# Kernel tuning notes

Hardware: AMD Instinct MI355X
Metric: run time of the kernel (lower is better)

The kernel has to match this reference:

```python
import jax, jax.numpy as jnp
import numpy as np

N = 500_000   # total nodes
D = 256       # in_dim
G = 1024      # num graphs (segments)
H = max(32, D // 2)  # gate hidden = 128
L = D // 2    # local pool dim = 128


def setup_inputs() -> dict:
    key = jax.random.key(0)
    ks = jax.random.split(key, 8)
    x = jax.random.normal(ks[0], (N, D), dtype=jnp.float32)
    batch = jnp.sort(jax.random.randint(ks[1], (N,), 0, G, dtype=jnp.int32))
    s = 0.02
    w1 = jax.random.normal(ks[2], (D, H), dtype=jnp.float32) * s
    b1 = jnp.zeros((H,), dtype=jnp.float32)
    w2 = jax.random.normal(ks[3], (H, 1), dtype=jnp.float32) * s
    b2 = jnp.zeros((1,), dtype=jnp.float32)
    lp_w = jax.random.normal(ks[4], (D, L), dtype=jnp.float32) * s
    lp_b = jnp.zeros((L,), dtype=jnp.float32)
    return {"x": x, "batch": batch, "w1": w1, "b1": b1, "w2": w2,
            "b2": b2, "lp_w": lp_w, "lp_b": lp_b}


def reference(x, batch, w1, b1, w2, b2, lp_w, lp_b):
    # segment counts (guard empty segments)
    ones = jnp.ones((x.shape[0],), dtype=x.dtype)
    cnt = jax.ops.segment_sum(ones, batch, num_segments=G)
    cnt = jnp.maximum(cnt, 1.0)[:, None]                      # [G,1]

    # mean pool
    mean_p = jax.ops.segment_sum(x, batch, num_segments=G) / cnt

    # max pool
    max_p = jax.ops.segment_max(x, batch, num_segments=G)

    # global attention pool: gate MLP -> per-segment softmax -> weighted sum
    # (Dropout is identity at inference.)
    h = jax.nn.gelu(x @ w1 + b1, approximate=False)           # [N,H]
    gate = (h @ w2 + b2)[:, 0]                                # [N]
    gmax = jax.ops.segment_max(gate, batch, num_segments=G)   # [G]
    e = jnp.exp(gate - gmax[batch])                           # [N]
    denom = jax.ops.segment_sum(e, batch, num_segments=G)     # [G]
    a = e / denom[batch]                                      # [N] softmax per graph
    att_p = jax.ops.segment_sum(a[:, None] * x, batch, num_segments=G)

    # local MLP pool then mean
    local = jax.nn.gelu(x @ lp_w + lp_b, approximate=False)   # [N,L]
    local_mean = jax.ops.segment_sum(local, batch, num_segments=G) / cnt

    return jnp.concatenate([mean_p, max_p, att_p, local_mean], axis=-1)  # [G, 3D + D//2]
```

## Files before the change

kernel.cpp:

```cpp
#include <hip/hip_runtime.h>
#include <hip/hip_bf16.h>
#include <float.h>
#include <math.h>


typedef __bf16 bf16;
typedef __bf16 bf16x8 __attribute__((ext_vector_type(8)));
typedef float f32x4 __attribute__((ext_vector_type(4)));

#define D 256
#define HDIM 128
#define LDIM 128
#define EBUF 768

__device__ __forceinline__ float gelu_f(float v) {
    return 0.5f * v * (1.0f + erff(v * 0.70710678118654752f));
}

__global__ __launch_bounds__(256) void k_prep(const float* __restrict__ w1,
                                              const float* __restrict__ lpw,
                                              bf16* __restrict__ w1T,
                                              bf16* __restrict__ lpT,
                                              float* __restrict__ local_sum,
                                              int G) {
    int t = blockIdx.x * 256 + threadIdx.x;
    if (t < G * LDIM) local_sum[t] = 0.0f;
    if (t < HDIM * D) {
        int n = t >> 8;
        int k = t & 255;
        w1T[t] = (bf16)w1[k * HDIM + n];
        lpT[t] = (bf16)lpw[k * LDIM + n];
    }
}

__global__ __launch_bounds__(256) void k_gate_local(
    const float* __restrict__ x, const int* __restrict__ batch,
    const bf16* __restrict__ w1T, const float* __restrict__ b1,
    const float* __restrict__ w2, const float* __restrict__ b2,
    const bf16* __restrict__ lpT, const float* __restrict__ lpb,
    float* __restrict__ gate, float* __restrict__ local_sum, int N)
{
    __shared__ bf16 xs[64][264];
    __shared__ int bs[64];
    __shared__ float gpart[4][64];

    const int tid  = threadIdx.x;
    const int wave = tid >> 6;
    const int lane = tid & 63;
    const int quad = lane >> 4;
    const int l16  = lane & 15;
    const long base = (long)blockIdx.x * 64;

    #pragma unroll
    for (int it = 0; it < 16; ++it) {
        int idx = it * 256 + tid;
        int row = idx >> 6;
        int c4  = idx & 63;
        long node = base + row;
        float4 v;
        if (node < N) v = *(const float4*)(x + node * D + c4 * 4);
        else          v = make_float4(0.f, 0.f, 0.f, 0.f);
        bf16* dst = &xs[row][c4 * 4];
        dst[0] = (bf16)v.x; dst[1] = (bf16)v.y; dst[2] = (bf16)v.z; dst[3] = (bf16)v.w;
    }
    if (tid < 64) bs[tid] = (base + tid < N) ? batch[base + tid] : 0x7fffffff;
    __syncthreads();

    const int c0 = wave * 32 + l16;
    const int c1 = c0 + 16;

    f32x4 zero = {0.f, 0.f, 0.f, 0.f};

    f32x4 acc0[4], acc1[4];
    #pragma unroll
    for (int mt = 0; mt < 4; ++mt) { acc0[mt] = zero; acc1[mt] = zero; }
    #pragma unroll
    for (int kt = 0; kt < 8; ++kt) {
        int k0 = kt * 32 + quad * 8;
        bf16x8 bfr0 = *(const bf16x8*)(w1T + c0 * D + k0);
        bf16x8 bfr1 = *(const bf16x8*)(w1T + c1 * D + k0);
        #pragma unroll
        for (int mt = 0; mt < 4; ++mt) {
            bf16x8 a = *(const bf16x8*)(&xs[mt * 16 + l16][k0]);
            acc0[mt] = __builtin_amdgcn_mfma_f32_16x16x32_bf16(a, bfr0, acc0[mt], 0, 0, 0);
            acc1[mt] = __builtin_amdgcn_mfma_f32_16x16x32_bf16(a, bfr1, acc1[mt], 0, 0, 0);
        }
    }

    {
        const float b1c0 = b1[c0], b1c1 = b1[c1];
        const float w2c0 = w2[c0], w2c1 = w2[c1];
        #pragma unroll
        for (int mt = 0; mt < 4; ++mt) {
            #pragma unroll
            for (int r = 0; r < 4; ++r) {
                float v = gelu_f(acc0[mt][r] + b1c0) * w2c0
                        + gelu_f(acc1[mt][r] + b1c1) * w2c1;
                v += __shfl_down(v, 8, 16);
                v += __shfl_down(v, 4, 16);
                v += __shfl_down(v, 2, 16);
                v += __shfl_down(v, 1, 16);
                if (l16 == 0) gpart[wave][mt * 16 + quad * 4 + r] = v;
            }
        }
    }
    __syncthreads();
    if (tid < 64) {
        long node = base + tid;
        if (node < N)
            gate[node] = gpart[0][tid] + gpart[1][tid] + gpart[2][tid] + gpart[3][tid] + b2[0];
    }

    #pragma unroll
    for (int mt = 0; mt < 4; ++mt) { acc0[mt] = zero; acc1[mt] = zero; }
    #pragma unroll
    for (int kt = 0; kt < 8; ++kt) {
        int k0 = kt * 32 + quad * 8;
        bf16x8 bfr0 = *(const bf16x8*)(lpT + c0 * D + k0);
        bf16x8 bfr1 = *(const bf16x8*)(lpT + c1 * D + k0);
        #pragma unroll
        for (int mt = 0; mt < 4; ++mt) {
            bf16x8 a = *(const bf16x8*)(&xs[mt * 16 + l16][k0]);
            acc0[mt] = __builtin_amdgcn_mfma_f32_16x16x32_bf16(a, bfr0, acc0[mt], 0, 0, 0);
            acc1[mt] = __builtin_amdgcn_mfma_f32_16x16x32_bf16(a, bfr1, acc1[mt], 0, 0, 0);
        }
    }

    const float lb0 = lpb[c0], lb1 = lpb[c1];
    const bool fast = (base + 63 < N) && (bs[0] == bs[63]);
    if (fast) {
        float s0 = 0.f, s1 = 0.f;
        #pragma unroll
        for (int mt = 0; mt < 4; ++mt) {
            #pragma unroll
            for (int r = 0; r < 4; ++r) {
                s0 += gelu_f(acc0[mt][r] + lb0);
                s1 += gelu_f(acc1[mt][r] + lb1);
            }
        }
        s0 += __shfl_xor(s0, 16); s0 += __shfl_xor(s0, 32);
        s1 += __shfl_xor(s1, 16); s1 += __shfl_xor(s1, 32);
        if (quad == 0) {
            int g = bs[0];
            atomicAdd(&local_sum[g * LDIM + c0], s0);
            atomicAdd(&local_sum[g * LDIM + c1], s1);
        }
    } else {
        int cur = -1;
        float s0 = 0.f, s1 = 0.f;
        #pragma unroll
        for (int mt = 0; mt < 4; ++mt) {
            #pragma unroll
            for (int r = 0; r < 4; ++r) {
                int lrow = mt * 16 + quad * 4 + r;
                if (base + lrow < N) {
                    int g = bs[lrow];
                    if (g != cur) {
                        if (cur >= 0) {
                            atomicAdd(&local_sum[cur * LDIM + c0], s0);
                            atomicAdd(&local_sum[cur * LDIM + c1], s1);
                        }
                        cur = g; s0 = 0.f; s1 = 0.f;
                    }
                    s0 += gelu_f(acc0[mt][r] + lb0);
                    s1 += gelu_f(acc1[mt][r] + lb1);
                }
            }
        }
        if (cur >= 0) {
            atomicAdd(&local_sum[cur * LDIM + c0], s0);
            atomicAdd(&local_sum[cur * LDIM + c1], s1);
        }
    }
}

__device__ __forceinline__ int lower_bound_i(const int* a, int n, int v) {
    int lo = 0, hi = n;
    while (lo < hi) { int mid = (lo + hi) >> 1; if (a[mid] < v) lo = mid + 1; else hi = mid; }
    return lo;
}

__global__ __launch_bounds__(256) void k_pool(
    const float* __restrict__ x, const int* __restrict__ batch,
    const float* __restrict__ gate, const float* __restrict__ local_sum,
    float* __restrict__ out, int N)
{
    const int g   = blockIdx.x;
    const int tid = threadIdx.x;
    const int wave = tid >> 6;
    const int lane = tid & 63;

    __shared__ int sse[2];
    __shared__ float wred[4];
    __shared__ float ebuf[EBUF];
    __shared__ float rsum[4][256];
    __shared__ float rmax[4][256];
    __shared__ float ratt[4][256];

    if (tid == 0) {
        sse[0] = lower_bound_i(batch, N, g);
        sse[1] = lower_bound_i(batch, N, g + 1);
    }
    __syncthreads();
    const int start = sse[0], end = sse[1];
    const int cnt = end - start;

    float m = -FLT_MAX;
    for (int i = start + tid; i < end; i += 256) m = fmaxf(m, gate[i]);
    #pragma unroll
    for (int off = 32; off > 0; off >>= 1) m = fmaxf(m, __shfl_xor(m, off));
    if (lane == 0) wred[wave] = m;
    __syncthreads();
    m = fmaxf(fmaxf(wred[0], wred[1]), fmaxf(wred[2], wred[3]));
    __syncthreads();

    const bool fits = (cnt <= EBUF);
    float dsum = 0.f;
    for (int i = start + tid; i < end; i += 256) {
        float e = expf(gate[i] - m);
        if (fits) ebuf[i - start] = e;
        dsum += e;
    }
    #pragma unroll
    for (int off = 32; off > 0; off >>= 1) dsum += __shfl_xor(dsum, off);
    __syncthreads();
    if (lane == 0) wred[wave] = dsum;
    __syncthreads();
    const float denom = wred[0] + wred[1] + wred[2] + wred[3];

    const int rg = tid >> 6;
    const int c4 = tid & 63;
    float sx = 0, sy = 0, sz = 0, sw = 0;
    float ax = 0, ay = 0, az = 0, aw = 0;
    float mx = -FLT_MAX, my = -FLT_MAX, mz = -FLT_MAX, mw = -FLT_MAX;
    for (int r0 = start; r0 < end; r0 += 4) {
        int r = r0 + rg;
        if (r < end) {
            float e = fits ? ebuf[r - start] : expf(gate[r] - m);
            float4 v = *(const float4*)(x + (long)r * D + c4 * 4);
            sx += v.x; sy += v.y; sz += v.z; sw += v.w;
            ax += e * v.x; ay += e * v.y; az += e * v.z; aw += e * v.w;
            mx = fmaxf(mx, v.x); my = fmaxf(my, v.y); mz = fmaxf(mz, v.z); mw = fmaxf(mw, v.w);
        }
    }
    const int cb = c4 * 4;
    rsum[rg][cb] = sx; rsum[rg][cb+1] = sy; rsum[rg][cb+2] = sz; rsum[rg][cb+3] = sw;
    ratt[rg][cb] = ax; ratt[rg][cb+1] = ay; ratt[rg][cb+2] = az; ratt[rg][cb+3] = aw;
    rmax[rg][cb] = mx; rmax[rg][cb+1] = my; rmax[rg][cb+2] = mz; rmax[rg][cb+3] = mw;
    __syncthreads();

    const float cntf = fmaxf((float)cnt, 1.0f);
    const float inv  = 1.0f / cntf;
    const float invd = (denom > 0.f) ? 1.0f / denom : 0.f;
    const long o = (long)g * 896;

    {
        int c = tid;
        float s  = rsum[0][c] + rsum[1][c] + rsum[2][c] + rsum[3][c];
        float a  = ratt[0][c] + ratt[1][c] + ratt[2][c] + ratt[3][c];
        float mm = fmaxf(fmaxf(rmax[0][c], rmax[1][c]), fmaxf(rmax[2][c], rmax[3][c]));
        if (cnt == 0) mm = -INFINITY;
        out[o + c]       = s * inv;
        out[o + 256 + c] = mm;
        out[o + 512 + c] = a * invd;
    }
    if (tid < 128) out[o + 768 + tid] = local_sum[g * LDIM + tid] * inv;
}

extern "C" void kernel_launch(void* const* d_in, const int* in_sizes, int n_in,
                              void* d_out, int out_size, void* d_ws, size_t ws_size,
                              hipStream_t stream) {
    const float* x   = (const float*)d_in[0];
    const int* batch = (const int*)d_in[1];
    const float* w1  = (const float*)d_in[2];
    const float* b1  = (const float*)d_in[3];
    const float* w2  = (const float*)d_in[4];
    const float* b2  = (const float*)d_in[5];
    const float* lpw = (const float*)d_in[6];
    const float* lpb = (const float*)d_in[7];
    float* out = (float*)d_out;

    const int N = in_sizes[0] / D;
    const int G = out_size / 896;

    char* ws = (char*)d_ws;
    size_t off = 0;
    float* gate = (float*)(ws + off); off += (((size_t)N * 4) + 255) & ~(size_t)255;
    bf16* w1T   = (bf16*)(ws + off);  off += (size_t)HDIM * D * 2;
    bf16* lpT   = (bf16*)(ws + off);  off += (size_t)LDIM * D * 2;
    float* local_sum = (float*)(ws + off); off += (size_t)G * LDIM * 4;

    const int prep_threads = G * LDIM;
    k_prep<<<(prep_threads + 255) / 256, 256, 0, stream>>>(w1, lpw, w1T, lpT, local_sum, G);
    k_gate_local<<<(int)((N + 63) / 64), 256, 0, stream>>>(x, batch, w1T, b1, w2, b2,
                                                           lpT, lpb, gate, local_sum, N);
    k_pool<<<G, 256, 0, stream>>>(x, batch, gate, local_sum, out, N);
}
```

Measured before the change: 916.7 us.

## Merge gate and local GEMMs, split pool into stats and column-halved pool kernels

```diff
diff --git a/kernel.cpp b/kernel.cpp
--- a/kernel.cpp
+++ b/kernel.cpp
@@ -5,13 +5,13 @@
 
 
 typedef __bf16 bf16;
+typedef __bf16 bf16x4 __attribute__((ext_vector_type(4)));
 typedef __bf16 bf16x8 __attribute__((ext_vector_type(8)));
 typedef float f32x4 __attribute__((ext_vector_type(4)));
 
 #define D 256
 #define HDIM 128
 #define LDIM 128
-#define EBUF 768
 
 __device__ __forceinline__ float gelu_f(float v) {
     return 0.5f * v * (1.0f + erff(v * 0.70710678118654752f));
@@ -22,8 +22,10 @@
                                               bf16* __restrict__ w1T,
                                               bf16* __restrict__ lpT,
                                               float* __restrict__ local_sum,
-                                              int G) {
+                                              int* __restrict__ segstart,
+                                              int G, int N) {
     int t = blockIdx.x * 256 + threadIdx.x;
+    if (t == 0) segstart[G] = N;
     if (t < G * LDIM) local_sum[t] = 0.0f;
     if (t < HDIM * D) {
         int n = t >> 8;
@@ -33,7 +35,7 @@
     }
 }
 
-__global__ __launch_bounds__(256) void k_gate_local(
+__global__ __launch_bounds__(256, 3) void k_gate_local(
     const float* __restrict__ x, const int* __restrict__ batch,
     const bf16* __restrict__ w1T, const float* __restrict__ b1,
     const float* __restrict__ w2, const float* __restrict__ b2,
@@ -60,8 +62,9 @@
         float4 v;
         if (node < N) v = *(const float4*)(x + node * D + c4 * 4);
         else          v = make_float4(0.f, 0.f, 0.f, 0.f);
-        bf16* dst = &xs[row][c4 * 4];
-        dst[0] = (bf16)v.x; dst[1] = (bf16)v.y; dst[2] = (bf16)v.z; dst[3] = (bf16)v.w;
+        bf16x4 pk;
+        pk[0] = (bf16)v.x; pk[1] = (bf16)v.y; pk[2] = (bf16)v.z; pk[3] = (bf16)v.w;
+        *(bf16x4*)(&xs[row][c4 * 4]) = pk;
     }
     if (tid < 64) bs[tid] = (base + tid < N) ? batch[base + tid] : 0x7fffffff;
     __syncthreads();
@@ -70,20 +73,24 @@
     const int c1 = c0 + 16;
 
     f32x4 zero = {0.f, 0.f, 0.f, 0.f};
-
-    f32x4 acc0[4], acc1[4];
-    #pragma unroll
-    for (int mt = 0; mt < 4; ++mt) { acc0[mt] = zero; acc1[mt] = zero; }
+    f32x4 h0[4], h1[4], l0[4], l1[4];
+    #pragma unroll
+    for (int mt = 0; mt < 4; ++mt) { h0[mt] = zero; h1[mt] = zero; l0[mt] = zero; l1[mt] = zero; }
+
     #pragma unroll
     for (int kt = 0; kt < 8; ++kt) {
         int k0 = kt * 32 + quad * 8;
-        bf16x8 bfr0 = *(const bf16x8*)(w1T + c0 * D + k0);
-        bf16x8 bfr1 = *(const bf16x8*)(w1T + c1 * D + k0);
+        bf16x8 bw0 = *(const bf16x8*)(w1T + c0 * D + k0);
+        bf16x8 bw1 = *(const bf16x8*)(w1T + c1 * D + k0);
+        bf16x8 bp0 = *(const bf16x8*)(lpT + c0 * D + k0);
+        bf16x8 bp1 = *(const bf16x8*)(lpT + c1 * D + k0);
         #pragma unroll
         for (int mt = 0; mt < 4; ++mt) {
             bf16x8 a = *(const bf16x8*)(&xs[mt * 16 + l16][k0]);
-            acc0[mt] = __builtin_amdgcn_mfma_f32_16x16x32_bf16(a, bfr0, acc0[mt], 0, 0, 0);
-            acc1[mt] = __builtin_amdgcn_mfma_f32_16x16x32_bf16(a, bfr1, acc1[mt], 0, 0, 0);
+            h0[mt] = __builtin_amdgcn_mfma_f32_16x16x32_bf16(a, bw0, h0[mt], 0, 0, 0);
+            h1[mt] = __builtin_amdgcn_mfma_f32_16x16x32_bf16(a, bw1, h1[mt], 0, 0, 0);
+            l0[mt] = __builtin_amdgcn_mfma_f32_16x16x32_bf16(a, bp0, l0[mt], 0, 0, 0);
+            l1[mt] = __builtin_amdgcn_mfma_f32_16x16x32_bf16(a, bp1, l1[mt], 0, 0, 0);
         }
     }
 
@@ -94,8 +101,8 @@
         for (int mt = 0; mt < 4; ++mt) {
             #pragma unroll
             for (int r = 0; r < 4; ++r) {
-                float v = gelu_f(acc0[mt][r] + b1c0) * w2c0
-                        + gelu_f(acc1[mt][r] + b1c1) * w2c1;
+                float v = gelu_f(h0[mt][r] + b1c0) * w2c0
+                        + gelu_f(h1[mt][r] + b1c1) * w2c1;
                 v += __shfl_down(v, 8, 16);
                 v += __shfl_down(v, 4, 16);
                 v += __shfl_down(v, 2, 16);
@@ -111,21 +118,6 @@
             gate[node] = gpart[0][tid] + gpart[1][tid] + gpart[2][tid] + gpart[3][tid] + b2[0];
     }
 
-    #pragma unroll
-    for (int mt = 0; mt < 4; ++mt) { acc0[mt] = zero; acc1[mt] = zero; }
-    #pragma unroll
-    for (int kt = 0; kt < 8; ++kt) {
-        int k0 = kt * 32 + quad * 8;
-        bf16x8 bfr0 = *(const bf16x8*)(lpT + c0 * D + k0);
-        bf16x8 bfr1 = *(const bf16x8*)(lpT + c1 * D + k0);
-        #pragma unroll
-        for (int mt = 0; mt < 4; ++mt) {
-            bf16x8 a = *(const bf16x8*)(&xs[mt * 16 + l16][k0]);
-            acc0[mt] = __builtin_amdgcn_mfma_f32_16x16x32_bf16(a, bfr0, acc0[mt], 0, 0, 0);
-            acc1[mt] = __builtin_amdgcn_mfma_f32_16x16x32_bf16(a, bfr1, acc1[mt], 0, 0, 0);
-        }
-    }
-
     const float lb0 = lpb[c0], lb1 = lpb[c1];
     const bool fast = (base + 63 < N) && (bs[0] == bs[63]);
     if (fast) {
@@ -134,8 +126,8 @@
         for (int mt = 0; mt < 4; ++mt) {
             #pragma unroll
             for (int r = 0; r < 4; ++r) {
-                s0 += gelu_f(acc0[mt][r] + lb0);
-                s1 += gelu_f(acc1[mt][r] + lb1);
+                s0 += gelu_f(l0[mt][r] + lb0);
+                s1 += gelu_f(l1[mt][r] + lb1);
             }
         }
         s0 += __shfl_xor(s0, 16); s0 += __shfl_xor(s0, 32);
@@ -162,8 +154,8 @@
                         }
                         cur = g; s0 = 0.f; s1 = 0.f;
                     }
-                    s0 += gelu_f(acc0[mt][r] + lb0);
-                    s1 += gelu_f(acc1[mt][r] + lb1);
+                    s0 += gelu_f(l0[mt][r] + lb0);
+                    s1 += gelu_f(l1[mt][r] + lb1);
                 }
             }
         }
@@ -180,10 +172,10 @@
     return lo;
 }
 
-__global__ __launch_bounds__(256) void k_pool(
-    const float* __restrict__ x, const int* __restrict__ batch,
-    const float* __restrict__ gate, const float* __restrict__ local_sum,
-    float* __restrict__ out, int N)
+__global__ __launch_bounds__(256) void k_stats(
+    const int* __restrict__ batch, const float* __restrict__ gate,
+    float* __restrict__ aw, float* __restrict__ segdenom,
+    int* __restrict__ segstart, int N)
 {
     const int g   = blockIdx.x;
     const int tid = threadIdx.x;
@@ -192,18 +184,12 @@
 
     __shared__ int sse[2];
     __shared__ float wred[4];
-    __shared__ float ebuf[EBUF];
-    __shared__ float rsum[4][256];
-    __shared__ float rmax[4][256];
-    __shared__ float ratt[4][256];
-
-    if (tid == 0) {
-        sse[0] = lower_bound_i(batch, N, g);
-        sse[1] = lower_bound_i(batch, N, g + 1);
-    }
+
+    if (tid == 0) sse[0] = lower_bound_i(batch, N, g);
+    if (tid == 1) sse[1] = lower_bound_i(batch, N, g + 1);
     __syncthreads();
     const int start = sse[0], end = sse[1];
-    const int cnt = end - start;
+    if (tid == 0) segstart[g] = start;
 
     float m = -FLT_MAX;
     for (int i = start + tid; i < end; i += 256) m = fmaxf(m, gate[i]);
@@ -214,57 +200,85 @@
     m = fmaxf(fmaxf(wred[0], wred[1]), fmaxf(wred[2], wred[3]));
     __syncthreads();
 
-    const bool fits = (cnt <= EBUF);
-    float dsum = 0.f;
+    float s = 0.f;
     for (int i = start + tid; i < end; i += 256) {
         float e = expf(gate[i] - m);
-        if (fits) ebuf[i - start] = e;
-        dsum += e;
-    }
-    #pragma unroll
-    for (int off = 32; off > 0; off >>= 1) dsum += __shfl_xor(dsum, off);
-    __syncthreads();
-    if (lane == 0) wred[wave] = dsum;
-    __syncthreads();
-    const float denom = wred[0] + wred[1] + wred[2] + wred[3];
-
-    const int rg = tid >> 6;
-    const int c4 = tid & 63;
+        aw[i] = e;
+        s += e;
+    }
+    #pragma unroll
+    for (int off = 32; off > 0; off >>= 1) s += __shfl_xor(s, off);
+    if (lane == 0) wred[wave] = s;
+    __syncthreads();
+    if (tid == 0) segdenom[g] = wred[0] + wred[1] + wred[2] + wred[3];
+}
+
+__global__ __launch_bounds__(256) void k_pool(
+    const float* __restrict__ x,
+    const float* __restrict__ aw, const float* __restrict__ segdenom,
+    const int* __restrict__ segstart, const float* __restrict__ local_sum,
+    float* __restrict__ out)
+{
+    const int g    = blockIdx.x >> 1;
+    const int half = blockIdx.x & 1;
+    const int tid  = threadIdx.x;
+    const int rg   = tid >> 5;
+    const int c4   = tid & 31;
+
+    __shared__ float psum[8][128];
+    __shared__ float pmax[8][128];
+    __shared__ float patt[8][128];
+
+    const int start = segstart[g];
+    const int end   = segstart[g + 1];
+    const int cnt   = end - start;
+
+    const float* xb = x + half * 128 + c4 * 4;
+
     float sx = 0, sy = 0, sz = 0, sw = 0;
-    float ax = 0, ay = 0, az = 0, aw = 0;
+    float ax = 0, ay = 0, az = 0, aw4 = 0;
     float mx = -FLT_MAX, my = -FLT_MAX, mz = -FLT_MAX, mw = -FLT_MAX;
-    for (int r0 = start; r0 < end; r0 += 4) {
-        int r = r0 + rg;
-        if (r < end) {
-            float e = fits ? ebuf[r - start] : expf(gate[r] - m);
-            float4 v = *(const float4*)(x + (long)r * D + c4 * 4);
-            sx += v.x; sy += v.y; sz += v.z; sw += v.w;
-            ax += e * v.x; ay += e * v.y; az += e * v.z; aw += e * v.w;
-            mx = fmaxf(mx, v.x); my = fmaxf(my, v.y); mz = fmaxf(mz, v.z); mw = fmaxf(mw, v.w);
-        }
-    }
+
+    int i = start + rg;
+    #define POOL_BODY(ri)                                                    \
+        {                                                                    \
+            float e = aw[ri];                                                \
+            float4 v = *(const float4*)(xb + (long)(ri) * D);                \
+            sx += v.x; sy += v.y; sz += v.z; sw += v.w;                      \
+            ax += e * v.x; ay += e * v.y; az += e * v.z; aw4 += e * v.w;     \
+            mx = fmaxf(mx, v.x); my = fmaxf(my, v.y);                        \
+            mz = fmaxf(mz, v.z); mw = fmaxf(mw, v.w);                        \
+        }
+    for (; i + 8 < end; i += 16) { POOL_BODY(i); POOL_BODY(i + 8); }
+    if (i < end) POOL_BODY(i);
+    #undef POOL_BODY
+
     const int cb = c4 * 4;
-    rsum[rg][cb] = sx; rsum[rg][cb+1] = sy; rsum[rg][cb+2] = sz; rsum[rg][cb+3] = sw;
-    ratt[rg][cb] = ax; ratt[rg][cb+1] = ay; ratt[rg][cb+2] = az; ratt[rg][cb+3] = aw;
-    rmax[rg][cb] = mx; rmax[rg][cb+1] = my; rmax[rg][cb+2] = mz; rmax[rg][cb+3] = mw;
-    __syncthreads();
-
-    const float cntf = fmaxf((float)cnt, 1.0f);
-    const float inv  = 1.0f / cntf;
-    const float invd = (denom > 0.f) ? 1.0f / denom : 0.f;
-    const long o = (long)g * 896;
-
-    {
+    psum[rg][cb] = sx; psum[rg][cb+1] = sy; psum[rg][cb+2] = sz; psum[rg][cb+3] = sw;
+    patt[rg][cb] = ax; patt[rg][cb+1] = ay; patt[rg][cb+2] = az; patt[rg][cb+3] = aw4;
+    pmax[rg][cb] = mx; pmax[rg][cb+1] = my; pmax[rg][cb+2] = mz; pmax[rg][cb+3] = mw;
+    __syncthreads();
+
+    const float inv  = 1.0f / fmaxf((float)cnt, 1.0f);
+    const float dn   = segdenom[g];
+    const float invd = (dn > 0.f) ? 1.0f / dn : 0.f;
+    const long  o    = (long)g * 896;
+
+    if (tid < 128) {
         int c = tid;
-        float s  = rsum[0][c] + rsum[1][c] + rsum[2][c] + rsum[3][c];
-        float a  = ratt[0][c] + ratt[1][c] + ratt[2][c] + ratt[3][c];
-        float mm = fmaxf(fmaxf(rmax[0][c], rmax[1][c]), fmaxf(rmax[2][c], rmax[3][c]));
+        float s = 0.f, a = 0.f, mm = -FLT_MAX;
+        #pragma unroll
+        for (int r = 0; r < 8; ++r) {
+            s += psum[r][c];
+            a += patt[r][c];
+            mm = fmaxf(mm, pmax[r][c]);
+        }
         if (cnt == 0) mm = -INFINITY;
-        out[o + c]       = s * inv;
-        out[o + 256 + c] = mm;
-        out[o + 512 + c] = a * invd;
-    }
-    if (tid < 128) out[o + 768 + tid] = local_sum[g * LDIM + tid] * inv;
+        out[o + half * 128 + c]       = s * inv;
+        out[o + 256 + half * 128 + c] = mm;
+        out[o + 512 + half * 128 + c] = a * invd;
+        if (half == 1) out[o + 768 + c] = local_sum[g * LDIM + c] * inv;
+    }
 }
 
 extern "C" void kernel_launch(void* const* d_in, const int* in_sizes, int n_in,
@@ -285,14 +299,19 @@
 
     char* ws = (char*)d_ws;
     size_t off = 0;
-    float* gate = (float*)(ws + off); off += (((size_t)N * 4) + 255) & ~(size_t)255;
-    bf16* w1T   = (bf16*)(ws + off);  off += (size_t)HDIM * D * 2;
-    bf16* lpT   = (bf16*)(ws + off);  off += (size_t)LDIM * D * 2;
+    float* gate      = (float*)(ws + off); off += (((size_t)N * 4) + 255) & ~(size_t)255;
+    float* aw        = (float*)(ws + off); off += (((size_t)N * 4) + 255) & ~(size_t)255;
+    bf16*  w1T       = (bf16*)(ws + off);  off += (size_t)HDIM * D * 2;
+    bf16*  lpT       = (bf16*)(ws + off);  off += (size_t)LDIM * D * 2;
     float* local_sum = (float*)(ws + off); off += (size_t)G * LDIM * 4;
+    float* segdenom  = (float*)(ws + off); off += (size_t)G * 4;
+    int*   segstart  = (int*)(ws + off);   off += (size_t)(G + 1) * 4;
 
     const int prep_threads = G * LDIM;
-    k_prep<<<(prep_threads + 255) / 256, 256, 0, stream>>>(w1, lpw, w1T, lpT, local_sum, G);
+    k_prep<<<(prep_threads + 255) / 256, 256, 0, stream>>>(w1, lpw, w1T, lpT, local_sum,
+                                                           segstart, G, N);
     k_gate_local<<<(int)((N + 63) / 64), 256, 0, stream>>>(x, batch, w1T, b1, w2, b2,
                                                            lpT, lpb, gate, local_sum, N);
-    k_pool<<<G, 256, 0, stream>>>(x, batch, gate, local_sum, out, N);
-}
+    k_stats<<<G, 256, 0, stream>>>(batch, gate, aw, segdenom, segstart, N);
+    k_pool<<<2 * G, 256, 0, stream>>>(x, aw, segdenom, segstart, local_sum, out);
+}
```

Measured after the change: 883.2 us. 3.7% less time.
